# Optimization experiments

Hardware: AMD Instinct MI355X
Metric: run time of the kernel (lower is better)

The kernel has to match this reference:

```python
import jax, jax.numpy as jnp
import numpy as np

B, S, I, C, N, V, O = 32, 256, 256, 512, 1024, 64, 256
EPS = 1e-12


def setup_inputs() -> dict:
    key = jax.random.key(0)
    ks = iter(jax.random.split(key, 40))

    def rn(shape, scale=0.05):
        return (jax.random.normal(next(ks), shape, jnp.float32) * scale)

    inp = {
        'x': jax.random.normal(next(ks), (B, S, I), jnp.float32),
        # LSTM controller (PyTorch gate order i,f,g,o)
        'lstm_Wih': rn((4 * C, I + V)), 'lstm_Whh': rn((4 * C, C)),
        'lstm_bih': rn((4 * C,)), 'lstm_bhh': rn((4 * C,)),
        # read head
        'r_key_W': rn((V, C)), 'r_key_b': rn((V,)),
        'r_str_W': rn((1, C)), 'r_str_b': rn((1,)),
        'r_gate_W': rn((1, C)), 'r_gate_b': rn((1,)),
        'r_shift_W': rn((3, C)), 'r_shift_b': rn((3,)),
        'r_gamma_W': rn((1, C)), 'r_gamma_b': rn((1,)),
        # write head (uses its own key/strength layers, plus erase/add)
        'w_key_W': rn((V, C)), 'w_key_b': rn((V,)),
        'w_str_W': rn((1, C)), 'w_str_b': rn((1,)),
        'w_erase_W': rn((V, C)), 'w_erase_b': rn((V,)),
        'w_add_W': rn((V, C)), 'w_add_b': rn((V,)),
        # output projection
        'out_W': rn((O, C + V)), 'out_b': rn((O,)),
    }
    return inp


def _lin(x, W, b):
    return x @ W.T + b


def _normalize(x, axis):
    n = jnp.linalg.norm(x, axis=axis, keepdims=True)
    return x / jnp.maximum(n, EPS)


def _content_addressing(key_vec, memory, strength):
    # key_vec: [B,V], memory: [B,N,V], strength: [B,1]
    kn = _normalize(key_vec, 1)
    mn = _normalize(memory, 2)
    sim = jnp.einsum('bv,bnv->bn', kn, mn)
    return jax.nn.softmax(strength * sim, axis=1)


def _ntm_forward(x, lstm_Wih, lstm_Whh, lstm_bih, lstm_bhh,
                 r_key_W, r_key_b, r_str_W, r_str_b, r_gate_W, r_gate_b,
                 r_shift_W, r_shift_b, r_gamma_W, r_gamma_b,
                 w_key_W, w_key_b, w_str_W, w_str_b,
                 w_erase_W, w_erase_b, w_add_W, w_add_b, out_W, out_b):
    b = x.shape[0]
    h0 = jnp.zeros((b, C), x.dtype)
    c0 = jnp.zeros((b, C), x.dtype)
    mem0 = jnp.zeros((b, N, V), x.dtype)
    rv0 = jnp.zeros((b, V), x.dtype)

    def step(carry, xt):
        h, c, memory, read_vec = carry
        # LSTM cell
        ci = jnp.concatenate([xt, read_vec], axis=1)          # [B, I+V]
        gates = _lin(ci, lstm_Wih, lstm_bih) + _lin(h, lstm_Whh, lstm_bhh)
        ig, fg, gg, og = jnp.split(gates, 4, axis=1)
        c = jax.nn.sigmoid(fg) * c + jax.nn.sigmoid(ig) * jnp.tanh(gg)
        h = jax.nn.sigmoid(og) * jnp.tanh(c)

        # read head
        key_r = jnp.tanh(_lin(h, r_key_W, r_key_b))
        str_r = jax.nn.softplus(_lin(h, r_str_W, r_str_b))
        gate = jax.nn.sigmoid(_lin(h, r_gate_W, r_gate_b))
        _shift = jax.nn.softmax(_lin(h, r_shift_W, r_shift_b), axis=1)  # computed but unused (as in source)
        gamma = 1.0 + jax.nn.softplus(_lin(h, r_gamma_W, r_gamma_b))
        cw = _content_addressing(key_r, memory, str_r)        # [B,N]
        sharp = cw ** gamma
        lw = sharp / jnp.sum(sharp, axis=1, keepdims=True)
        fw = gate * lw + (1.0 - gate) * cw
        read_vec = jnp.einsum('bn,bnv->bv', fw, memory)

        # write head (erase then add)
        key_w = jnp.tanh(_lin(h, w_key_W, w_key_b))
        str_w = jax.nn.softplus(_lin(h, w_str_W, w_str_b))
        ww = _content_addressing(key_w, memory, str_w)        # [B,N]
        erase = jax.nn.sigmoid(_lin(h, w_erase_W, w_erase_b))  # [B,V]
        add = jnp.tanh(_lin(h, w_add_W, w_add_b))              # [B,V]
        memory = memory * (1.0 - ww[:, :, None] * erase[:, None, :]) \
                 + ww[:, :, None] * add[:, None, :]

        out = _lin(jnp.concatenate([h, read_vec], axis=1), out_W, out_b)
        return (h, c, memory, read_vec), out

    (_, _, final_memory, _), outs = jax.lax.scan(
        step, (h0, c0, mem0, rv0), jnp.swapaxes(x, 0, 1))
    return jnp.swapaxes(outs, 0, 1), final_memory


def reference(x, lstm_Wih, lstm_Whh, lstm_bih, lstm_bhh,
              r_key_W, r_key_b, r_str_W, r_str_b, r_gate_W, r_gate_b,
              r_shift_W, r_shift_b, r_gamma_W, r_gamma_b,
              w_key_W, w_key_b, w_str_W, w_str_b,
              w_erase_W, w_erase_b, w_add_W, w_add_b, out_W, out_b):
    return _ntm_forward(x, lstm_Wih, lstm_Whh, lstm_bih, lstm_bhh,
                        r_key_W, r_key_b, r_str_W, r_str_b, r_gate_W, r_gate_b,
                        r_shift_W, r_shift_b, r_gamma_W, r_gamma_b,
                        w_key_W, w_key_b, w_str_W, w_str_b,
                        w_erase_W, w_erase_b, w_add_W, w_add_b, out_W, out_b)
```

## Files before the change

kernel.cpp:

```cpp
#include <hip/hip_runtime.h>

#define Bv 32
#define Sv 256
#define Iv 256
#define Cv 512
#define Nv 1024
#define Vv 64
#define Ov 256
#define NBLK 256
#define NTHR 256

#define CLAIM_I(x)   ((x)*8)
#define GAL_I(x,q)   (64 + ((x)*4+(q))*8)
#define XROOT_I(x)   (320 + (x)*8)
#define ZERO_BYTES   (640*4)
#define FBASE 1024
#define HBU(x,t1,bb)  (FBASE + (x)*2048 + (t1)*1024 + (bb)*256)
#define EGU(x,bb,k)   (FBASE + 16384 + (x)*2048 + (bb)*512 + (k)*64)
#define SUMPF(x,bb,k) (FBASE + 32768 + (x)*128 + (bb)*32 + (k)*4)
#define HPF(x,bb,r)   (FBASE + 33792 + (((x)*4+(bb))*32 + (r))*264)

struct KP {
  const float *x, *Wih, *Whh, *bih, *bhh;
  const float *rkW, *rkb, *rsW, *rsb, *rgW, *rgb, *rgammaW, *rgammab;
  const float *wkW, *wkb, *wsW, *wsb, *weW, *web, *waW, *wab;
  const float *outW, *outb;
  float *out;
  float *memout;
  float *ws;
};

typedef _Float16 half2v __attribute__((ext_vector_type(2)));
union HU { unsigned u; half2v h; };

__device__ inline float sigf(float x){ return 1.f/(1.f+expf(-x)); }
__device__ inline float softplusf(float x){ return fmaxf(x,0.f) + log1pf(expf(-fabsf(x))); }
__device__ inline unsigned packh(float a, float b){
  HU z; z.h = half2v{(_Float16)a, (_Float16)b}; return z.u;
}
__device__ inline float h2lo(unsigned u){ HU z; z.u = u; return (float)z.h.x; }
__device__ inline float h2hi(unsigned u){ HU z; z.u = u; return (float)z.h.y; }
__device__ inline float dot2(unsigned w, unsigned a, float acc){
  HU wu, au; wu.u = w; au.u = a;
  return __builtin_amdgcn_fdot2(wu.h, au.h, acc, false);
}

__device__ inline void stg_f(float* p, float v){
  asm volatile("global_store_dword %0, %1, off sc0" :: "v"(p), "v"(v) : "memory");
}
__device__ inline void stg_u(unsigned* p, unsigned v){
  asm volatile("global_store_dword %0, %1, off sc0" :: "v"(p), "v"(v) : "memory");
}
#define LDG4U(dst, addr) asm volatile("global_load_dwordx4 %0, %1, off sc0" : "=v"(dst) : "v"(addr) : "memory")
#define LDG4F(dst, addr) asm volatile("global_load_dwordx4 %0, %1, off sc0" : "=v"(dst) : "v"(addr) : "memory")
#define LDGU(dst, addr)  asm volatile("global_load_dword %0, %1, off sc0"  : "=v"(dst) : "v"(addr) : "memory")
#define LDGF(dst, addr)  asm volatile("global_load_dword %0, %1, off sc0"  : "=v"(dst) : "v"(addr) : "memory")
#define WAITV do { asm volatile("s_waitcnt vmcnt(0)" ::: "memory"); __builtin_amdgcn_sched_barrier(0); } while(0)

#define AADD(p,v) __hip_atomic_fetch_add((p),(v),__ATOMIC_RELAXED,__HIP_MEMORY_SCOPE_AGENT)
#define ALD(p)    __hip_atomic_load((p),__ATOMIC_RELAXED,__HIP_MEMORY_SCOPE_AGENT)

#define SPIN(cond_expr) do { unsigned sp = 0; \
  while (cond_expr){ __builtin_amdgcn_s_sleep(2); \
    if (((++sp)&1023u)==0u && (__builtin_amdgcn_s_memrealtime()-t0) > 300000000ULL) break; } } while(0)

__device__ inline float headact(int o, float s){
  if (o < 64)  return tanhf(s);
  if (o == 64) return softplusf(s);
  if (o == 65) return sigf(s);
  if (o == 66) return 1.f + softplusf(s);
  if (o < 131) return tanhf(s);
  if (o == 131) return softplusf(s);
  if (o < 196) return sigf(s);
  return tanhf(s);
}
__device__ inline void head_src(const KP& P, int o, const float** row, float* bias){
  if (o < 64)       { *row = P.rkW + o*Cv;        *bias = P.rkb[o]; }
  else if (o == 64) { *row = P.rsW;               *bias = P.rsb[0]; }
  else if (o == 65) { *row = P.rgW;               *bias = P.rgb[0]; }
  else if (o == 66) { *row = P.rgammaW;           *bias = P.rgammab[0]; }
  else if (o < 131) { *row = P.wkW + (o-67)*Cv;   *bias = P.wkb[o-67]; }
  else if (o == 131){ *row = P.wsW;               *bias = P.wsb[0]; }
  else if (o < 196) { *row = P.weW + (o-132)*Cv;  *bias = P.web[o-132]; }
  else              { *row = P.waW + (o-196)*Cv;  *bias = P.wab[o-196]; }
}

__global__ __launch_bounds__(NTHR) void ntm_kernel(KP P){
  __shared__ unsigned Wg[64][420];
  __shared__ unsigned actL[4][420];
  __shared__ float memL[128][66];
  __shared__ float gb[64][4];
  __shared__ float biasL[64];
  __shared__ float htmpf[16][5];
  __shared__ float headsL[264];
  __shared__ float knr[64], knw[64];
  __shared__ float scal[8];
  __shared__ float erL2[128], egL2[128], ewL[128];
  __shared__ float red[32][9];
  __shared__ float red2[2][4];
  __shared__ float sumS1[4][8][4];
  __shared__ float cEL[4], cGL[4];
  __shared__ float sumS4[8][4];
  __shared__ float rvpE[4][64], rvpG[4][64];
  __shared__ float rvfinE[64], rvfinG[64];
  __shared__ int sXcd, sRank;

  const int tid = threadIdx.x;
  float* wsf = P.ws;
  unsigned* wsu = (unsigned*)P.ws;
  int* wsi = (int*)P.ws;
  const unsigned long long t0 = __builtin_amdgcn_s_memrealtime();

  if (tid == 0){
    unsigned xcc;
    asm volatile("s_getreg_b32 %0, hwreg(20, 0, 32)" : "=s"(xcc));
    int xc = (int)(xcc & 7u);
    int rk = AADD(&wsi[CLAIM_I(xc)], 1);
    sXcd = xc; sRank = rk & 31;
  }
  __syncthreads();
  const int xcd = sXcd, rank = sRank;
  const int bl_own = rank >> 3;
  const int rk8 = rank & 7;
  const int bglob = xcd*4 + bl_own;

  for (int idx = tid; idx < 64*416; idx += NTHR){
    int rl = idx / 416, u = idx % 416;
    int gr = (rl>>4)*Cv + rank*16 + (rl&15);
    int c0 = 2*u;
    float a, b2;
    if (c0 < 320){ a = P.Wih[gr*320 + c0]; b2 = P.Wih[gr*320 + c0 + 1]; }
    else { int q = c0 - 320; a = P.Whh[gr*512 + q]; b2 = P.Whh[gr*512 + q + 1]; }
    Wg[rl][u] = packh(a, b2);
  }
  if (tid < 64){
    int gr = (tid>>4)*Cv + rank*16 + (tid&15);
    biasL[tid] = P.bih[gr] + P.bhh[gr];
  }
  float wA[16], wB[16], bA, bB;
  {
    const float* rowA; head_src(P, tid, &rowA, &bA);
    #pragma unroll
    for (int j = 0; j < 16; ++j) wA[j] = rowA[rank*16 + j];
    const float* rowB; head_src(P, 256 + (tid & 3), &rowB, &bB);
    #pragma unroll
    for (int j = 0; j < 16; ++j) wB[j] = rowB[rank*16 + j];
  }
  for (int idx = tid; idx < 128*66; idx += NTHR) ((float*)memL)[idx] = 0.f;
  __syncthreads();

  float cS = 0.f;
  int gs = 0;

  for (int t = 0; t < Sv; ++t){
    {
      int bb = tid>>6, part = tid&63;
      const float* xp = P.x + ((size_t)(xcd*4+bb)*Sv + (size_t)t)*Iv + part*4;
      float4 xv = *(const float4*)xp;
      actL[bb][part*2]   = packh(xv.x, xv.y);
      actL[bb][part*2+1] = packh(xv.z, xv.w);
      if (t > 0){
        uint4 hq;
        unsigned e0,e1,e2,e3,e4,e5,e6,e7,g0,g1,g2,g3,g4,g5,g6,g7;
        float4 sv = {0,0,0,0};
        int b2 = tid>>5, j = tid&31;
        LDG4U(hq, wsu + HBU(xcd,(t+1)&1,bb) + part*4);
        if (tid < 128){
          const unsigned* eb = wsu + EGU(xcd,b2,0) + j;
          LDGU(e0,eb+0*64); LDGU(e1,eb+1*64); LDGU(e2,eb+2*64); LDGU(e3,eb+3*64);
          LDGU(e4,eb+4*64); LDGU(e5,eb+5*64); LDGU(e6,eb+6*64); LDGU(e7,eb+7*64);
          const unsigned* ggb = eb + 32;
          LDGU(g0,ggb+0*64); LDGU(g1,ggb+1*64); LDGU(g2,ggb+2*64); LDGU(g3,ggb+3*64);
          LDGU(g4,ggb+4*64); LDGU(g5,ggb+5*64); LDGU(g6,ggb+6*64); LDGU(g7,ggb+7*64);
        }
        if (tid < 32){ LDG4F(sv, wsf + SUMPF(xcd, tid>>3, tid&7)); }
        WAITV;
        *(uint4*)&actL[bb][160 + part*4] = hq;
        if (tid < 32) *(float4*)&sumS1[tid>>3][tid&7][0] = sv;
        __syncthreads();
        if (tid < 4){
          float Se = 0.f, Sg = 0.f;
          #pragma unroll
          for (int k2 = 0; k2 < 8; ++k2){ Se += sumS1[tid][k2][0]; Sg += sumS1[tid][k2][1]; }
          float g = sumS1[tid][0][3];
          cEL[tid] = (1.f - g)/Se;
          cGL[tid] = g/Sg;
        }
        __syncthreads();
        if (tid < 128){
          float Elo = h2lo(e0)+h2lo(e1)+h2lo(e2)+h2lo(e3)+h2lo(e4)+h2lo(e5)+h2lo(e6)+h2lo(e7);
          float Ehi = h2hi(e0)+h2hi(e1)+h2hi(e2)+h2hi(e3)+h2hi(e4)+h2hi(e5)+h2hi(e6)+h2hi(e7);
          float Glo = h2lo(g0)+h2lo(g1)+h2lo(g2)+h2lo(g3)+h2lo(g4)+h2lo(g5)+h2lo(g6)+h2lo(g7);
          float Ghi = h2hi(g0)+h2hi(g1)+h2hi(g2)+h2hi(g3)+h2hi(g4)+h2hi(g5)+h2hi(g6)+h2hi(g7);
          actL[b2][128 + j] = packh(cGL[b2]*Glo + cEL[b2]*Elo, cGL[b2]*Ghi + cEL[b2]*Ehi);
        }
      } else {
        for (int idx = tid; idx < 4*288; idx += NTHR){
          int bb2 = idx/288, u = 128 + idx%288;
          actL[bb2][u] = 0u;
        }
      }
    }
    __syncthreads();
    {
      int g = tid>>6, l = tid&63, rr = l>>2, bb = l&3, row = g*16+rr;
      const unsigned* wr = &Wg[row][0];
      const unsigned* ar = &actL[bb][0];
      float a0 = biasL[row], a1 = 0.f, a2 = 0.f, a3 = 0.f;
      #pragma unroll 13
      for (int u = 0; u < 416; u += 8){
        uint4 w0 = *(const uint4*)(wr+u);
        uint4 v0 = *(const uint4*)(ar+u);
        uint4 w1 = *(const uint4*)(wr+u+4);
        uint4 v1 = *(const uint4*)(ar+u+4);
        a0 = dot2(w0.x, v0.x, a0); a1 = dot2(w0.y, v0.y, a1);
        a2 = dot2(w0.z, v0.z, a2); a3 = dot2(w0.w, v0.w, a3);
        a0 = dot2(w1.x, v1.x, a0); a1 = dot2(w1.y, v1.y, a1);
        a2 = dot2(w1.z, v1.z, a2); a3 = dot2(w1.w, v1.w, a3);
      }
      gb[row][bb] = (a0+a1)+(a2+a3);
    }
    __syncthreads();
    if (tid < 64){
      int j = tid>>2, bb = tid&3;
      float ig = gb[j][bb], fg = gb[16+j][bb], gg = gb[32+j][bb], og = gb[48+j][bb];
      cS = sigf(fg)*cS + sigf(ig)*tanhf(gg);
      htmpf[j][bb] = sigf(og)*tanhf(cS);
    }
    __syncthreads();
    if (tid < 32){
      int pr = tid>>2, bb = tid&3;
      stg_u(wsu + HBU(xcd,t&1,bb) + rank*8 + pr, packh(htmpf[2*pr][bb], htmpf[2*pr+1][bb]));
    }
    {
      float p0=0.f,p1=0.f,p2=0.f,p3=0.f,q0=0.f,q1=0.f,q2=0.f,q3=0.f;
      #pragma unroll
      for (int j = 0; j < 16; ++j){
        float h0=htmpf[j][0], h1=htmpf[j][1], h2=htmpf[j][2], h3=htmpf[j][3];
        p0+=wA[j]*h0; p1+=wA[j]*h1; p2+=wA[j]*h2; p3+=wA[j]*h3;
        q0+=wB[j]*h0; q1+=wB[j]*h1; q2+=wB[j]*h2; q3+=wB[j]*h3;
      }
      stg_f(wsf + HPF(xcd,0,rank) + tid, p0);
      stg_f(wsf + HPF(xcd,1,rank) + tid, p1);
      stg_f(wsf + HPF(xcd,2,rank) + tid, p2);
      stg_f(wsf + HPF(xcd,3,rank) + tid, p3);
      if (tid < 4){
        int o2 = 256 + tid;
        stg_f(wsf + HPF(xcd,0,rank) + o2, q0);
        stg_f(wsf + HPF(xcd,1,rank) + o2, q1);
        stg_f(wsf + HPF(xcd,2,rank) + o2, q2);
        stg_f(wsf + HPF(xcd,3,rank) + o2, q3);
      }
    }
    WAITV;
    __syncthreads();
    if (tid == 0){
      int a = AADD(&wsi[GAL_I(xcd, rank>>3)], 1);
      if (a == 8*(gs+1) - 1) AADD(&wsi[XROOT_I(xcd)], 1);
    }
    if (t > 0){
      int oo = tid>>3, kc = tid&7;
      int o = rk8*32 + oo;
      const float* wrow = P.outW + o*576 + kc*72;
      const unsigned* ab = &actL[bl_own][0];
      float p = 0.f;
      if (kc < 7){
        int u0 = 160 + kc*36;
        #pragma unroll 9
        for (int i = 0; i < 36; ++i){
          unsigned u = ab[u0+i];
          p += h2lo(u)*wrow[2*i] + h2hi(u)*wrow[2*i+1];
        }
      } else {
        #pragma unroll
        for (int i = 0; i < 4; ++i){
          unsigned u = ab[412+i];
          p += h2lo(u)*wrow[2*i] + h2hi(u)*wrow[2*i+1];
        }
        #pragma unroll 8
        for (int i = 0; i < 32; ++i){
          unsigned u = ab[128+i];
          p += h2lo(u)*wrow[8+2*i] + h2hi(u)*wrow[9+2*i];
        }
      }
      red[oo][kc] = p;
      __syncthreads();
      if (tid < 32){
        int o2 = rk8*32 + tid;
        float s = P.outb[o2];
        #pragma unroll
        for (int k2 = 0; k2 < 8; ++k2) s += red[tid][k2];
        P.out[((size_t)bglob*Sv + (t-1))*Ov + o2] = s;
      }
    }
    if (tid == 0){ SPIN(ALD(&wsi[XROOT_I(xcd)]) < 4*(gs+1)); }
    __syncthreads();
    ++gs;

    {
      float s = bA, s2 = bB;
      #pragma unroll
      for (int rr = 0; rr < 4; ++rr){
        const float* hb = wsf + HPF(xcd, bl_own, rr*8);
        float a0,a1,a2,a3,a4,a5,a6,a7,b0,b1,b2,b3,b4,b5,b6,b7;
        int o2 = 256 + (tid & 3);
        LDGF(a0, hb + 0*264 + tid); LDGF(a1, hb + 1*264 + tid);
        LDGF(a2, hb + 2*264 + tid); LDGF(a3, hb + 3*264 + tid);
        LDGF(a4, hb + 4*264 + tid); LDGF(a5, hb + 5*264 + tid);
        LDGF(a6, hb + 6*264 + tid); LDGF(a7, hb + 7*264 + tid);
        LDGF(b0, hb + 0*264 + o2);  LDGF(b1, hb + 1*264 + o2);
        LDGF(b2, hb + 2*264 + o2);  LDGF(b3, hb + 3*264 + o2);
        LDGF(b4, hb + 4*264 + o2);  LDGF(b5, hb + 5*264 + o2);
        LDGF(b6, hb + 6*264 + o2);  LDGF(b7, hb + 7*264 + o2);
        WAITV;
        s  += ((a0+a1)+(a2+a3))+((a4+a5)+(a6+a7));
        s2 += ((b0+b1)+(b2+b3))+((b4+b5)+(b6+b7));
      }
      headsL[tid] = headact(tid, s);
      if (tid < 4) headsL[256+tid] = headact(256+tid, s2);
    }
    __syncthreads();
    if (tid < 64){
      float kr = headsL[tid], kw = headsL[67+tid];
      float sr = kr*kr, sw2 = kw*kw;
      #pragma unroll
      for (int off = 32; off; off >>= 1){ sr += __shfl_xor(sr, off); sw2 += __shfl_xor(sw2, off); }
      knr[tid] = kr * (1.f/fmaxf(sqrtf(sr), 1e-12f));
      knw[tid] = kw * (1.f/fmaxf(sqrtf(sw2), 1e-12f));
    }
    __syncthreads();
    {
      float str_r = headsL[64], gamma = headsL[66], str_w = headsL[131];
      float er = 0.f, eg = 0.f, ew = 0.f;
      if (tid < 128){
        float dr = 0.f, dw = 0.f, nn = 0.f;
        #pragma unroll 8
        for (int v = 0; v < 64; ++v){
          float m = memL[tid][v];
          dr += m*knr[v]; dw += m*knw[v]; nn += m*m;
        }
        float innm = 1.f/fmaxf(sqrtf(nn), 1e-12f);
        float tr = str_r*(dr*innm - 1.f);
        er = expf(tr);
        eg = expf(gamma*tr);
        ew = expf(str_w*(dw*innm - 1.f));
        erL2[tid] = er; egL2[tid] = eg; ewL[tid] = ew;
      }
      float s0 = er, s1 = eg, s2 = ew;
      #pragma unroll
      for (int off = 32; off; off >>= 1){
        s0 += __shfl_xor(s0, off); s1 += __shfl_xor(s1, off); s2 += __shfl_xor(s2, off);
      }
      if ((tid & 63) == 0 && tid < 128){
        int wv = tid>>6; red2[wv][0] = s0; red2[wv][1] = s1; red2[wv][2] = s2;
      }
      __syncthreads();
      if (tid == 0){
        float* sp = wsf + SUMPF(xcd,bl_own,rk8);
        stg_f(sp+0, red2[0][0]+red2[1][0]);
        stg_f(sp+1, red2[0][1]+red2[1][1]);
        stg_f(sp+2, red2[0][2]+red2[1][2]);
        stg_f(sp+3, headsL[65]);
      }
    }
    {
      int v = tid & 63, cc = tid >> 6;
      float pE = 0.f, pG = 0.f;
      #pragma unroll 8
      for (int j = 0; j < 32; ++j){
        int r = cc*32 + j;
        float m = memL[r][v];
        pE += erL2[r]*m; pG += egL2[r]*m;
      }
      rvpE[cc][v] = pE; rvpG[cc][v] = pG;
    }
    __syncthreads();
    if (tid < 64){
      rvfinE[tid] = rvpE[0][tid]+rvpE[1][tid]+rvpE[2][tid]+rvpE[3][tid];
      rvfinG[tid] = rvpG[0][tid]+rvpG[1][tid]+rvpG[2][tid]+rvpG[3][tid];
    }
    __syncthreads();
    if (tid < 32)
      stg_u(wsu + EGU(xcd,bl_own,rk8) + tid, packh(rvfinE[2*tid], rvfinE[2*tid+1]));
    else if (tid < 64)
      stg_u(wsu + EGU(xcd,bl_own,rk8) + tid, packh(rvfinG[2*(tid-32)], rvfinG[2*(tid-32)+1]));
    WAITV;
    __syncthreads();
    if (tid == 0){
      int a = AADD(&wsi[GAL_I(xcd, rank>>3)], 1);
      if (a == 8*(gs+1) - 1) AADD(&wsi[XROOT_I(xcd)], 1);
      SPIN(ALD(&wsi[XROOT_I(xcd)]) < 4*(gs+1));
    }
    __syncthreads();
    ++gs;

    {
      float4 sv = {0,0,0,0};
      if (tid < 8){ LDG4F(sv, wsf + SUMPF(xcd,bl_own,tid)); }
      WAITV;
      if (tid < 8){ *(float4*)&sumS4[tid][0] = sv; }
    }
    __syncthreads();
    if (tid == 0){
      float Sw = 0.f;
      #pragma unroll
      for (int k2 = 0; k2 < 8; ++k2) Sw += sumS4[k2][2];
      scal[6] = Sw;
    }
    __syncthreads();
    {
      float rSw = 1.f/scal[6];
      #pragma unroll 4
      for (int e2 = 0; e2 < 32; ++e2){
        int flat = tid + e2*256;
        int r = flat >> 6, v2 = flat & 63;
        float ww = ewL[r]*rSw;
        memL[r][v2] = memL[r][v2]*(1.f - ww*headsL[132+v2]) + ww*headsL[196+v2];
      }
    }
    __syncthreads();
  }

  {
    int bb = tid>>6, part = tid&63;
    uint4 hq;
    unsigned e0,e1,e2,e3,e4,e5,e6,e7,g0,g1,g2,g3,g4,g5,g6,g7;
    float4 sv = {0,0,0,0};
    int b2 = tid>>5, j = tid&31;
    LDG4U(hq, wsu + HBU(xcd,(Sv-1)&1,bb) + part*4);
    if (tid < 128){
      const unsigned* eb = wsu + EGU(xcd,b2,0) + j;
      LDGU(e0,eb+0*64); LDGU(e1,eb+1*64); LDGU(e2,eb+2*64); LDGU(e3,eb+3*64);
      LDGU(e4,eb+4*64); LDGU(e5,eb+5*64); LDGU(e6,eb+6*64); LDGU(e7,eb+7*64);
      const unsigned* ggb = eb + 32;
      LDGU(g0,ggb+0*64); LDGU(g1,ggb+1*64); LDGU(g2,ggb+2*64); LDGU(g3,ggb+3*64);
      LDGU(g4,ggb+4*64); LDGU(g5,ggb+5*64); LDGU(g6,ggb+6*64); LDGU(g7,ggb+7*64);
    }
    if (tid < 32){ LDG4F(sv, wsf + SUMPF(xcd, tid>>3, tid&7)); }
    WAITV;
    *(uint4*)&actL[bb][160 + part*4] = hq;
    if (tid < 32) *(float4*)&sumS1[tid>>3][tid&7][0] = sv;
    __syncthreads();
    if (tid < 4){
      float Se = 0.f, Sg = 0.f;
      #pragma unroll
      for (int k2 = 0; k2 < 8; ++k2){ Se += sumS1[tid][k2][0]; Sg += sumS1[tid][k2][1]; }
      float g = sumS1[tid][0][3];
      cEL[tid] = (1.f - g)/Se;
      cGL[tid] = g/Sg;
    }
    __syncthreads();
    if (tid < 128){
      float Elo = h2lo(e0)+h2lo(e1)+h2lo(e2)+h2lo(e3)+h2lo(e4)+h2lo(e5)+h2lo(e6)+h2lo(e7);
      float Ehi = h2hi(e0)+h2hi(e1)+h2hi(e2)+h2hi(e3)+h2hi(e4)+h2hi(e5)+h2hi(e6)+h2hi(e7);
      float Glo = h2lo(g0)+h2lo(g1)+h2lo(g2)+h2lo(g3)+h2lo(g4)+h2lo(g5)+h2lo(g6)+h2lo(g7);
      float Ghi = h2hi(g0)+h2hi(g1)+h2hi(g2)+h2hi(g3)+h2hi(g4)+h2hi(g5)+h2hi(g6)+h2hi(g7);
      actL[b2][128 + j] = packh(cGL[b2]*Glo + cEL[b2]*Elo, cGL[b2]*Ghi + cEL[b2]*Ehi);
    }
  }
  __syncthreads();
  {
    int oo = tid>>3, kc = tid&7;
    int o = rk8*32 + oo;
    const float* wrow = P.outW + o*576 + kc*72;
    const unsigned* ab = &actL[bl_own][0];
    float p = 0.f;
    if (kc < 7){
      int u0 = 160 + kc*36;
      #pragma unroll 9
      for (int i = 0; i < 36; ++i){
        unsigned u = ab[u0+i];
        p += h2lo(u)*wrow[2*i] + h2hi(u)*wrow[2*i+1];
      }
    } else {
      #pragma unroll
      for (int i = 0; i < 4; ++i){
        unsigned u = ab[412+i];
        p += h2lo(u)*wrow[2*i] + h2hi(u)*wrow[2*i+1];
      }
      #pragma unroll 8
      for (int i = 0; i < 32; ++i){
        unsigned u = ab[128+i];
        p += h2lo(u)*wrow[8+2*i] + h2hi(u)*wrow[9+2*i];
      }
    }
    red[oo][kc] = p;
    __syncthreads();
    if (tid < 32){
      int o2 = rk8*32 + tid;
      float s = P.outb[o2];
      #pragma unroll
      for (int k2 = 0; k2 < 8; ++k2) s += red[tid][k2];
      P.out[((size_t)bglob*Sv + (Sv-1))*Ov + o2] = s;
    }
  }
  for (int e2 = 0; e2 < 32; ++e2){
    int flat = tid + e2*256;
    int r = flat >> 6, v2 = flat & 63;
    P.memout[((size_t)bglob*Nv + (size_t)rk8*128 + r)*Vv + v2] = memL[r][v2];
  }
}

extern "C" void kernel_launch(void* const* d_in, const int* in_sizes, int n_in,
                              void* d_out, int out_size, void* d_ws, size_t ws_size,
                              hipStream_t stream) {
  (void)in_sizes; (void)n_in; (void)out_size; (void)ws_size;
  KP p;
  p.x       = (const float*)d_in[0];
  p.Wih     = (const float*)d_in[1];
  p.Whh     = (const float*)d_in[2];
  p.bih     = (const float*)d_in[3];
  p.bhh     = (const float*)d_in[4];
  p.rkW     = (const float*)d_in[5];  p.rkb     = (const float*)d_in[6];
  p.rsW     = (const float*)d_in[7];  p.rsb     = (const float*)d_in[8];
  p.rgW     = (const float*)d_in[9];  p.rgb     = (const float*)d_in[10];
  p.rgammaW = (const float*)d_in[13]; p.rgammab = (const float*)d_in[14];
  p.wkW     = (const float*)d_in[15]; p.wkb     = (const float*)d_in[16];
  p.wsW     = (const float*)d_in[17]; p.wsb     = (const float*)d_in[18];
  p.weW     = (const float*)d_in[19]; p.web     = (const float*)d_in[20];
  p.waW     = (const float*)d_in[21]; p.wab     = (const float*)d_in[22];
  p.outW    = (const float*)d_in[23]; p.outb    = (const float*)d_in[24];
  p.out     = (float*)d_out;
  p.memout  = (float*)d_out + (size_t)Bv*Sv*Ov;
  p.ws      = (float*)d_ws;

  hipMemsetAsync(d_ws, 0, ZERO_BYTES, stream);
  hipLaunchKernelGGL(ntm_kernel, dim3(NBLK), dim3(NTHR), 0, stream, p);
}
```

Before: 4.596 ms.

## Double block threads and split LSTM gate dot products across two halves

Raises the threads per block from 256 to 512. The LSTM gate matvec is split along K into two halves whose partial sums are combined in shared memory, and the read-vector and memory-update loops are spread over twice as many threads. Other phases are guarded to the first 256 threads. The aim is to shorten the per-step critical path of this latency-bound recurrent kernel, at the cost of more register pressure, an extra reduction step and idle threads in the guarded phases.

```diff
diff --git a/kernel.cpp b/kernel.cpp
--- a/kernel.cpp
+++ b/kernel.cpp
@@ -8,7 +8,7 @@
 #define Vv 64
 #define Ov 256
 #define NBLK 256
-#define NTHR 256
+#define NTHR 512
 
 #define CLAIM_I(x)   ((x)*8)
 #define GAL_I(x,q)   (64 + ((x)*4+(q))*8)
@@ -89,7 +89,7 @@
   __shared__ unsigned Wg[64][420];
   __shared__ unsigned actL[4][420];
   __shared__ float memL[128][66];
-  __shared__ float gb[64][4];
+  __shared__ float gbp[64][4][2];
   __shared__ float biasL[64];
   __shared__ float htmpf[16][5];
   __shared__ float headsL[264];
@@ -101,7 +101,7 @@
   __shared__ float sumS1[4][8][4];
   __shared__ float cEL[4], cGL[4];
   __shared__ float sumS4[8][4];
-  __shared__ float rvpE[4][64], rvpG[4][64];
+  __shared__ float rvpE[8][64], rvpG[8][64];
   __shared__ float rvfinE[64], rvfinG[64];
   __shared__ int sXcd, sRank;
 
@@ -137,8 +137,8 @@
     int gr = (tid>>4)*Cv + rank*16 + (tid&15);
     biasL[tid] = P.bih[gr] + P.bhh[gr];
   }
-  float wA[16], wB[16], bA, bB;
-  {
+  float wA[16], wB[16], bA = 0.f, bB = 0.f;
+  if (tid < 256){
     const float* rowA; head_src(P, tid, &rowA, &bA);
     #pragma unroll
     for (int j = 0; j < 16; ++j) wA[j] = rowA[rank*16 + j];
@@ -154,17 +154,17 @@
 
   for (int t = 0; t < Sv; ++t){
     {
-      int bb = tid>>6, part = tid&63;
-      const float* xp = P.x + ((size_t)(xcd*4+bb)*Sv + (size_t)t)*Iv + part*4;
-      float4 xv = *(const float4*)xp;
-      actL[bb][part*2]   = packh(xv.x, xv.y);
-      actL[bb][part*2+1] = packh(xv.z, xv.w);
+      int bb = tid>>7, part = tid&127;
+      const float* xp = P.x + ((size_t)(xcd*4+bb)*Sv + (size_t)t)*Iv + part*2;
+      float2 xv = *(const float2*)xp;
+      actL[bb][part] = packh(xv.x, xv.y);
       if (t > 0){
-        uint4 hq;
-        unsigned e0,e1,e2,e3,e4,e5,e6,e7,g0,g1,g2,g3,g4,g5,g6,g7;
+        uint4 hq = {};
+        unsigned e0=0,e1=0,e2=0,e3=0,e4=0,e5=0,e6=0,e7=0,g0=0,g1=0,g2=0,g3=0,g4=0,g5=0,g6=0,g7=0;
         float4 sv = {0,0,0,0};
+        int hb2 = tid>>6, hpart = tid&63;
         int b2 = tid>>5, j = tid&31;
-        LDG4U(hq, wsu + HBU(xcd,(t+1)&1,bb) + part*4);
+        if (tid < 256){ LDG4U(hq, wsu + HBU(xcd,(t+1)&1,hb2) + hpart*4); }
         if (tid < 128){
           const unsigned* eb = wsu + EGU(xcd,b2,0) + j;
           LDGU(e0,eb+0*64); LDGU(e1,eb+1*64); LDGU(e2,eb+2*64); LDGU(e3,eb+3*64);
@@ -175,7 +175,7 @@
         }
         if (tid < 32){ LDG4F(sv, wsf + SUMPF(xcd, tid>>3, tid&7)); }
         WAITV;
-        *(uint4*)&actL[bb][160 + part*4] = hq;
+        if (tid < 256){ *(uint4*)&actL[hb2][160 + hpart*4] = hq; }
         if (tid < 32) *(float4*)&sumS1[tid>>3][tid&7][0] = sv;
         __syncthreads();
         if (tid < 4){
@@ -203,12 +203,14 @@
     }
     __syncthreads();
     {
-      int g = tid>>6, l = tid&63, rr = l>>2, bb = l&3, row = g*16+rr;
+      int half = tid>>8, l = tid&255;
+      int g = l>>6, ll = l&63, rr = ll>>2, bb = ll&3, row = g*16+rr;
       const unsigned* wr = &Wg[row][0];
       const unsigned* ar = &actL[bb][0];
-      float a0 = biasL[row], a1 = 0.f, a2 = 0.f, a3 = 0.f;
+      int u0 = half*208;
+      float a0 = (half==0) ? biasL[row] : 0.f, a1 = 0.f, a2 = 0.f, a3 = 0.f;
       #pragma unroll 13
-      for (int u = 0; u < 416; u += 8){
+      for (int u = u0; u < u0+208; u += 8){
         uint4 w0 = *(const uint4*)(wr+u);
         uint4 v0 = *(const uint4*)(ar+u);
         uint4 w1 = *(const uint4*)(wr+u+4);
@@ -218,12 +220,15 @@
         a0 = dot2(w1.x, v1.x, a0); a1 = dot2(w1.y, v1.y, a1);
         a2 = dot2(w1.z, v1.z, a2); a3 = dot2(w1.w, v1.w, a3);
       }
-      gb[row][bb] = (a0+a1)+(a2+a3);
+      gbp[row][bb][half] = (a0+a1)+(a2+a3);
     }
     __syncthreads();
     if (tid < 64){
       int j = tid>>2, bb = tid&3;
-      float ig = gb[j][bb], fg = gb[16+j][bb], gg = gb[32+j][bb], og = gb[48+j][bb];
+      float ig = gbp[j][bb][0]    + gbp[j][bb][1];
+      float fg = gbp[16+j][bb][0] + gbp[16+j][bb][1];
+      float gg = gbp[32+j][bb][0] + gbp[32+j][bb][1];
+      float og = gbp[48+j][bb][0] + gbp[48+j][bb][1];
       cS = sigf(fg)*cS + sigf(ig)*tanhf(gg);
       htmpf[j][bb] = sigf(og)*tanhf(cS);
     }
@@ -232,7 +237,7 @@
       int pr = tid>>2, bb = tid&3;
       stg_u(wsu + HBU(xcd,t&1,bb) + rank*8 + pr, packh(htmpf[2*pr][bb], htmpf[2*pr+1][bb]));
     }
-    {
+    if (tid < 256){
       float p0=0.f,p1=0.f,p2=0.f,p3=0.f,q0=0.f,q1=0.f,q2=0.f,q3=0.f;
       #pragma unroll
       for (int j = 0; j < 16; ++j){
@@ -259,31 +264,33 @@
       if (a == 8*(gs+1) - 1) AADD(&wsi[XROOT_I(xcd)], 1);
     }
     if (t > 0){
-      int oo = tid>>3, kc = tid&7;
-      int o = rk8*32 + oo;
-      const float* wrow = P.outW + o*576 + kc*72;
-      const unsigned* ab = &actL[bl_own][0];
-      float p = 0.f;
-      if (kc < 7){
-        int u0 = 160 + kc*36;
-        #pragma unroll 9
-        for (int i = 0; i < 36; ++i){
-          unsigned u = ab[u0+i];
-          p += h2lo(u)*wrow[2*i] + h2hi(u)*wrow[2*i+1];
-        }
-      } else {
-        #pragma unroll
-        for (int i = 0; i < 4; ++i){
-          unsigned u = ab[412+i];
-          p += h2lo(u)*wrow[2*i] + h2hi(u)*wrow[2*i+1];
-        }
-        #pragma unroll 8
-        for (int i = 0; i < 32; ++i){
-          unsigned u = ab[128+i];
-          p += h2lo(u)*wrow[8+2*i] + h2hi(u)*wrow[9+2*i];
-        }
-      }
-      red[oo][kc] = p;
+      if (tid < 256){
+        int oo = tid>>3, kc = tid&7;
+        int o = rk8*32 + oo;
+        const float* wrow = P.outW + o*576 + kc*72;
+        const unsigned* ab = &actL[bl_own][0];
+        float p = 0.f;
+        if (kc < 7){
+          int u0 = 160 + kc*36;
+          #pragma unroll 9
+          for (int i = 0; i < 36; ++i){
+            unsigned u = ab[u0+i];
+            p += h2lo(u)*wrow[2*i] + h2hi(u)*wrow[2*i+1];
+          }
+        } else {
+          #pragma unroll
+          for (int i = 0; i < 4; ++i){
+            unsigned u = ab[412+i];
+            p += h2lo(u)*wrow[2*i] + h2hi(u)*wrow[2*i+1];
+          }
+          #pragma unroll 8
+          for (int i = 0; i < 32; ++i){
+            unsigned u = ab[128+i];
+            p += h2lo(u)*wrow[8+2*i] + h2hi(u)*wrow[9+2*i];
+          }
+        }
+        red[oo][kc] = p;
+      }
       __syncthreads();
       if (tid < 32){
         int o2 = rk8*32 + tid;
@@ -297,7 +304,7 @@
     __syncthreads();
     ++gs;
 
-    {
+    if (tid < 256){
       float s = bA, s2 = bB;
       #pragma unroll
       for (int rr = 0; rr < 4; ++rr){
@@ -367,8 +374,8 @@
       int v = tid & 63, cc = tid >> 6;
       float pE = 0.f, pG = 0.f;
       #pragma unroll 8
-      for (int j = 0; j < 32; ++j){
-        int r = cc*32 + j;
+      for (int j = 0; j < 16; ++j){
+        int r = cc*16 + j;
         float m = memL[r][v];
         pE += erL2[r]*m; pG += egL2[r]*m;
       }
@@ -376,8 +383,10 @@
     }
     __syncthreads();
     if (tid < 64){
-      rvfinE[tid] = rvpE[0][tid]+rvpE[1][tid]+rvpE[2][tid]+rvpE[3][tid];
-      rvfinG[tid] = rvpG[0][tid]+rvpG[1][tid]+rvpG[2][tid]+rvpG[3][tid];
+      float e = 0.f, g = 0.f;
+      #pragma unroll
+      for (int c2 = 0; c2 < 8; ++c2){ e += rvpE[c2][tid]; g += rvpG[c2][tid]; }
+      rvfinE[tid] = e; rvfinG[tid] = g;
     }
     __syncthreads();
     if (tid < 32)
@@ -411,8 +420,8 @@
     {
       float rSw = 1.f/scal[6];
       #pragma unroll 4
-      for (int e2 = 0; e2 < 32; ++e2){
-        int flat = tid + e2*256;
+      for (int e2 = 0; e2 < 16; ++e2){
+        int flat = tid + e2*512;
         int r = flat >> 6, v2 = flat & 63;
         float ww = ewL[r]*rSw;
         memL[r][v2] = memL[r][v2]*(1.f - ww*headsL[132+v2]) + ww*headsL[196+v2];
@@ -422,12 +431,12 @@
   }
 
   {
-    int bb = tid>>6, part = tid&63;
-    uint4 hq;
-    unsigned e0,e1,e2,e3,e4,e5,e6,e7,g0,g1,g2,g3,g4,g5,g6,g7;
+    uint4 hq = {};
+    unsigned e0=0,e1=0,e2=0,e3=0,e4=0,e5=0,e6=0,e7=0,g0=0,g1=0,g2=0,g3=0,g4=0,g5=0,g6=0,g7=0;
     float4 sv = {0,0,0,0};
+    int hb2 = tid>>6, hpart = tid&63;
     int b2 = tid>>5, j = tid&31;
-    LDG4U(hq, wsu + HBU(xcd,(Sv-1)&1,bb) + part*4);
+    if (tid < 256){ LDG4U(hq, wsu + HBU(xcd,(Sv-1)&1,hb2) + hpart*4); }
     if (tid < 128){
       const unsigned* eb = wsu + EGU(xcd,b2,0) + j;
       LDGU(e0,eb+0*64); LDGU(e1,eb+1*64); LDGU(e2,eb+2*64); LDGU(e3,eb+3*64);
@@ -438,7 +447,7 @@
     }
     if (tid < 32){ LDG4F(sv, wsf + SUMPF(xcd, tid>>3, tid&7)); }
     WAITV;
-    *(uint4*)&actL[bb][160 + part*4] = hq;
+    if (tid < 256){ *(uint4*)&actL[hb2][160 + hpart*4] = hq; }
     if (tid < 32) *(float4*)&sumS1[tid>>3][tid&7][0] = sv;
     __syncthreads();
     if (tid < 4){
@@ -460,31 +469,33 @@
   }
   __syncthreads();
   {
-    int oo = tid>>3, kc = tid&7;
-    int o = rk8*32 + oo;
-    const float* wrow = P.outW + o*576 + kc*72;
-    const unsigned* ab = &actL[bl_own][0];
-    float p = 0.f;
-    if (kc < 7){
-      int u0 = 160 + kc*36;
-      #pragma unroll 9
-      for (int i = 0; i < 36; ++i){
-        unsigned u = ab[u0+i];
-        p += h2lo(u)*wrow[2*i] + h2hi(u)*wrow[2*i+1];
-      }
-    } else {
-      #pragma unroll
-      for (int i = 0; i < 4; ++i){
-        unsigned u = ab[412+i];
-        p += h2lo(u)*wrow[2*i] + h2hi(u)*wrow[2*i+1];
-      }
-      #pragma unroll 8
-      for (int i = 0; i < 32; ++i){
-        unsigned u = ab[128+i];
-        p += h2lo(u)*wrow[8+2*i] + h2hi(u)*wrow[9+2*i];
-      }
-    }
-    red[oo][kc] = p;
+    if (tid < 256){
+      int oo = tid>>3, kc = tid&7;
+      int o = rk8*32 + oo;
+      const float* wrow = P.outW + o*576 + kc*72;
+      const unsigned* ab = &actL[bl_own][0];
+      float p = 0.f;
+      if (kc < 7){
+        int u0 = 160 + kc*36;
+        #pragma unroll 9
+        for (int i = 0; i < 36; ++i){
+          unsigned u = ab[u0+i];
+          p += h2lo(u)*wrow[2*i] + h2hi(u)*wrow[2*i+1];
+        }
+      } else {
+        #pragma unroll
+        for (int i = 0; i < 4; ++i){
+          unsigned u = ab[412+i];
+          p += h2lo(u)*wrow[2*i] + h2hi(u)*wrow[2*i+1];
+        }
+        #pragma unroll 8
+        for (int i = 0; i < 32; ++i){
+          unsigned u = ab[128+i];
+          p += h2lo(u)*wrow[8+2*i] + h2hi(u)*wrow[9+2*i];
+        }
+      }
+      red[oo][kc] = p;
+    }
     __syncthreads();
     if (tid < 32){
       int o2 = rk8*32 + tid;
@@ -494,8 +505,8 @@
       P.out[((size_t)bglob*Sv + (Sv-1))*Ov + o2] = s;
     }
   }
-  for (int e2 = 0; e2 < 32; ++e2){
-    int flat = tid + e2*256;
+  for (int e2 = 0; e2 < 16; ++e2){
+    int flat = tid + e2*512;
     int r = flat >> 6, v2 = flat & 63;
     P.memout[((size_t)bglob*Nv + (size_t)rk8*128 + r)*Vv + v2] = memL[r][v2];
   }
```

Result: slower. 5.878 ms (+27.9%).

## Keep LSTM gate weights in registers and split K across wave quarters

Applied to the files above, without the earlier changes.

Moves the per-block packed half-precision LSTM gate weight slice out of shared memory into 26 uint4 registers per thread. Each thread now owns one gate row and a quarter of the reduction dimension for all four batches, and partial sums are combined through a small shared buffer in the activation step. This is meant to cut the shared-memory weight reads in the per-timestep matvec, leaving only activation reads, which are broadcast. The cost is 104 extra VGPRs per thread, which may cause spills, plus an extra cross-quarter reduction.

```diff
diff --git a/kernel.cpp b/kernel.cpp
--- a/kernel.cpp
+++ b/kernel.cpp
@@ -86,10 +86,9 @@
 }
 
 __global__ __launch_bounds__(NTHR) void ntm_kernel(KP P){
-  __shared__ unsigned Wg[64][420];
   __shared__ unsigned actL[4][420];
   __shared__ float memL[128][66];
-  __shared__ float gb[64][4];
+  __shared__ float gbq[4][4][68];
   __shared__ float biasL[64];
   __shared__ float htmpf[16][5];
   __shared__ float headsL[264];
@@ -124,20 +123,30 @@
   const int rk8 = rank & 7;
   const int bglob = xcd*4 + bl_own;
 
-  for (int idx = tid; idx < 64*416; idx += NTHR){
-    int rl = idx / 416, u = idx % 416;
-    int gr = (rl>>4)*Cv + rank*16 + (rl&15);
-    int c0 = 2*u;
-    float a, b2;
-    if (c0 < 320){ a = P.Wih[gr*320 + c0]; b2 = P.Wih[gr*320 + c0 + 1]; }
-    else { int q = c0 - 320; a = P.Whh[gr*512 + q]; b2 = P.Whh[gr*512 + q + 1]; }
-    Wg[rl][u] = packh(a, b2);
+  const int qw = tid >> 6;
+  const int rw = tid & 63;
+  const int grw = (rw>>4)*Cv + rank*16 + (rw&15);
+  uint4 wreg[26];
+  {
+    #pragma unroll
+    for (int jj = 0; jj < 26; ++jj){
+      unsigned uu[4];
+      #pragma unroll
+      for (int c = 0; c < 4; ++c){
+        int e = qw*208 + 8*jj + 2*c;
+        float2 w2;
+        if (e < 320) w2 = *(const float2*)(P.Wih + grw*320 + e);
+        else         w2 = *(const float2*)(P.Whh + grw*512 + (e-320));
+        uu[c] = packh(w2.x, w2.y);
+      }
+      wreg[jj].x = uu[0]; wreg[jj].y = uu[1]; wreg[jj].z = uu[2]; wreg[jj].w = uu[3];
+    }
   }
   if (tid < 64){
     int gr = (tid>>4)*Cv + rank*16 + (tid&15);
     biasL[tid] = P.bih[gr] + P.bhh[gr];
   }
-  float wA[16], wB[16], bA, bB;
+  float wA[16], wB[16], bA = 0.f, bB = 0.f;
   {
     const float* rowA; head_src(P, tid, &rowA, &bA);
     #pragma unroll
@@ -203,27 +212,32 @@
     }
     __syncthreads();
     {
-      int g = tid>>6, l = tid&63, rr = l>>2, bb = l&3, row = g*16+rr;
-      const unsigned* wr = &Wg[row][0];
-      const unsigned* ar = &actL[bb][0];
-      float a0 = biasL[row], a1 = 0.f, a2 = 0.f, a3 = 0.f;
-      #pragma unroll 13
-      for (int u = 0; u < 416; u += 8){
-        uint4 w0 = *(const uint4*)(wr+u);
-        uint4 v0 = *(const uint4*)(ar+u);
-        uint4 w1 = *(const uint4*)(wr+u+4);
-        uint4 v1 = *(const uint4*)(ar+u+4);
-        a0 = dot2(w0.x, v0.x, a0); a1 = dot2(w0.y, v0.y, a1);
-        a2 = dot2(w0.z, v0.z, a2); a3 = dot2(w0.w, v0.w, a3);
-        a0 = dot2(w1.x, v1.x, a0); a1 = dot2(w1.y, v1.y, a1);
-        a2 = dot2(w1.z, v1.z, a2); a3 = dot2(w1.w, v1.w, a3);
-      }
-      gb[row][bb] = (a0+a1)+(a2+a3);
+      const int base0 = qw*104;
+      float a00=0.f,a01=0.f,a10=0.f,a11=0.f,a20=0.f,a21=0.f,a30=0.f,a31=0.f;
+      #pragma unroll
+      for (int jj = 0; jj < 26; ++jj){
+        uint4 w = wreg[jj];
+        uint4 v0 = *(const uint4*)&actL[0][base0+4*jj];
+        uint4 v1 = *(const uint4*)&actL[1][base0+4*jj];
+        uint4 v2 = *(const uint4*)&actL[2][base0+4*jj];
+        uint4 v3 = *(const uint4*)&actL[3][base0+4*jj];
+        a00=dot2(w.x,v0.x,a00); a01=dot2(w.y,v0.y,a01); a00=dot2(w.z,v0.z,a00); a01=dot2(w.w,v0.w,a01);
+        a10=dot2(w.x,v1.x,a10); a11=dot2(w.y,v1.y,a11); a10=dot2(w.z,v1.z,a10); a11=dot2(w.w,v1.w,a11);
+        a20=dot2(w.x,v2.x,a20); a21=dot2(w.y,v2.y,a21); a20=dot2(w.z,v2.z,a20); a21=dot2(w.w,v2.w,a21);
+        a30=dot2(w.x,v3.x,a30); a31=dot2(w.y,v3.y,a31); a30=dot2(w.z,v3.z,a30); a31=dot2(w.w,v3.w,a31);
+      }
+      gbq[qw][0][rw] = a00+a01;
+      gbq[qw][1][rw] = a10+a11;
+      gbq[qw][2][rw] = a20+a21;
+      gbq[qw][3][rw] = a30+a31;
     }
     __syncthreads();
     if (tid < 64){
       int j = tid>>2, bb = tid&3;
-      float ig = gb[j][bb], fg = gb[16+j][bb], gg = gb[32+j][bb], og = gb[48+j][bb];
+      float ig = biasL[j]    + gbq[0][bb][j]    + gbq[1][bb][j]    + gbq[2][bb][j]    + gbq[3][bb][j];
+      float fg = biasL[16+j] + gbq[0][bb][16+j] + gbq[1][bb][16+j] + gbq[2][bb][16+j] + gbq[3][bb][16+j];
+      float gg = biasL[32+j] + gbq[0][bb][32+j] + gbq[1][bb][32+j] + gbq[2][bb][32+j] + gbq[3][bb][32+j];
+      float og = biasL[48+j] + gbq[0][bb][48+j] + gbq[1][bb][48+j] + gbq[2][bb][48+j] + gbq[3][bb][48+j];
       cS = sigf(fg)*cS + sigf(ig)*tanhf(gg);
       htmpf[j][bb] = sigf(og)*tanhf(cS);
     }
```

Result: faster. 4.245 ms (-7.7%).
